# Kernel optimization log

Hardware: AMD Instinct MI355X
Metric: run time of the kernel (lower is better)

The kernel has to match this reference:

```python
import jax, jax.numpy as jnp
import numpy as np

B, T, C, H = 4, 2048, 1024, 16


def setup_inputs() -> dict:
    key = jax.random.key(0)
    k0, k1, k2 = jax.random.split(key, 3)
    s = C ** -0.5
    return {
        "x": jax.random.normal(k0, (B, T, C), jnp.float32),
        "Wqkv": jax.random.normal(k1, (C, 3 * C), jnp.float32) * s,
        "bqkv": jnp.zeros((3 * C,), jnp.float32),
        "Wo": jax.random.normal(k2, (C, C), jnp.float32) * s,
        "bo": jnp.zeros((C,), jnp.float32),
        "decoder": 1,
    }


def reference(x, Wqkv, bqkv, Wo, bo, decoder):
    Bx, Tx, Cx = x.shape
    d = Cx // H  # head dim
    qkv = x @ Wqkv + bqkv  # [B,T,3C]
    q, k, v = jnp.split(qkv, 3, axis=-1)
    q = q.reshape(Bx, Tx, H, d).transpose(0, 2, 1, 3)  # [B,H,T,d]
    k = k.reshape(Bx, Tx, H, d).transpose(0, 2, 1, 3)
    v = v.reshape(Bx, Tx, H, d).transpose(0, 2, 1, 3)
    # Source: qk / embd_dim**(-0.5)  ==  qk * sqrt(embd_dim)  (faithful quirk)
    scale = jnp.asarray(Cx ** 0.5, x.dtype)
    qk = jnp.einsum("bhqd,bhkd->bhqk", q, k) * scale  # [B,H,T,T]
    if decoder:  # decoder is a Python int constant
        tril = jnp.tril(jnp.ones((Tx, Tx), bool))
        qk = jnp.where(tril, qk, -jnp.inf)
    attn = jax.nn.softmax(qk, axis=-1)
    out = jnp.einsum("bhqk,bhkd->bhqd", attn, v)  # [B,H,T,d]
    out = out.transpose(0, 2, 1, 3).reshape(Bx, Tx, Cx)
    return out @ Wo + bo
```

## Files before the change

kernel.cpp:

```cpp
#include <hip/hip_runtime.h>
#include <cstdint>
#include <cstddef>

#define T_SEQ 2048
#define CEMB  1024
#define NHEAD 16
#define DHEAD 64

#define QSCALE 46.1662413084468f

typedef __attribute__((ext_vector_type(8))) short bf16x8;
typedef __attribute__((ext_vector_type(4))) float f32x4;

static __device__ __forceinline__ unsigned short f2bf(float x) {
    unsigned u = __builtin_bit_cast(unsigned, x);
    unsigned r = (u + 0x7FFFu + ((u >> 16) & 1u)) >> 16;
    return (unsigned short)r;
}
static __device__ __forceinline__ float bf2f(unsigned short b) {
    unsigned u = ((unsigned)b) << 16;
    return __builtin_bit_cast(float, u);
}

static __device__ __forceinline__ void gload16(const short* gsrc, short* ldsbase) {
    __builtin_amdgcn_global_load_lds(
        (const __attribute__((address_space(1))) void*)gsrc,
        (__attribute__((address_space(3))) void*)ldsbase, 16, 0, 0);
}

__global__ __launch_bounds__(256) void split_x_kernel(
    const float* __restrict__ x, short* __restrict__ hi, short* __restrict__ lo)
{
    size_t base = ((size_t)blockIdx.x * 256 + threadIdx.x) * 8;
    float4 f0 = *(const float4*)(x + base);
    float4 f1 = *(const float4*)(x + base + 4);
    float xs[8] = {f0.x, f0.y, f0.z, f0.w, f1.x, f1.y, f1.z, f1.w};
    bf16x8 h8, l8;
    #pragma unroll
    for (int e = 0; e < 8; ++e) {
        unsigned u = __builtin_bit_cast(unsigned, xs[e]);
        h8[e] = (short)(unsigned short)(u >> 16);
        float hf = __builtin_bit_cast(float, u & 0xFFFF0000u);
        l8[e] = (short)f2bf(xs[e] - hf);
    }
    *(bf16x8*)(hi + base) = h8;
    *(bf16x8*)(lo + base) = l8;
}

template<int SPLIT, int OUT_MODE>
__global__ __launch_bounds__(256) void gemm_mfma_kernel(
    const short* __restrict__ Ah, const short* __restrict__ Al,
    const short* __restrict__ Bh, const short* __restrict__ Bl,
    const float* __restrict__ bias,
    void* __restrict__ Cout, void* __restrict__ Cout2, int K, int ldc)
{
    __shared__ __align__(16) short smem[(SPLIT == 3) ? 16384 : 8192];

    const int tid = threadIdx.x;
    const int w = tid >> 6, l = tid & 63;
    const int lr = l & 15, lg = l >> 4;
    const int wr = w >> 1, wc = w & 1;
    const int row0 = blockIdx.y * 128;
    const int col0 = blockIdx.x * 128;

    f32x4 acc[4][4];
    #pragma unroll
    for (int mt = 0; mt < 4; ++mt)
        #pragma unroll
        for (int nt = 0; nt < 4; ++nt)
            acc[mt][nt] = (f32x4){0.f, 0.f, 0.f, 0.f};

    const int s0 = w * 128 + l, s1 = s0 + 64;
    const size_t aoff0 = (size_t)(row0 + (s0 & 127)) * K + (s0 >> 7) * 8;
    const size_t aoff1 = (size_t)(row0 + (s1 & 127)) * K + (s1 >> 7) * 8;
    const size_t boff0 = (size_t)(col0 + (s0 & 127)) * K + (s0 >> 7) * 8;
    const size_t boff1 = (size_t)(col0 + (s1 & 127)) * K + (s1 >> 7) * 8;
    const short* gA0 = Ah + aoff0;  const short* gA1 = Ah + aoff1;
    const short* gB0 = Bh + boff0;  const short* gB1 = Bh + boff1;
    const short* gAl0 = nullptr; const short* gAl1 = nullptr;
    const short* gBl0 = nullptr; const short* gBl1 = nullptr;
    if constexpr (SPLIT == 3) {
        gAl0 = Al + aoff0;  gAl1 = Al + aoff1;
        gBl0 = Bl + boff0;  gBl1 = Bl + boff1;
    }
    short* const dA0 = &smem[(w * 128) * 8];
    short* const dA1 = &smem[(w * 128 + 64) * 8];
    short* const dB0 = &smem[4096 + (w * 128) * 8];
    short* const dB1 = &smem[4096 + (w * 128 + 64) * 8];

    for (int kt = 0; kt < K; kt += 32) {
        __syncthreads();
        gload16(gA0 + kt, dA0);
        gload16(gA1 + kt, dA1);
        gload16(gB0 + kt, dB0);
        gload16(gB1 + kt, dB1);
        if constexpr (SPLIT == 3) {
            gload16(gAl0 + kt, dA0 + 8192);
            gload16(gAl1 + kt, dA1 + 8192);
            gload16(gBl0 + kt, dB0 + 8192);
            gload16(gBl1 + kt, dB1 + 8192);
        }
        __syncthreads();

        const int ao = (lg * 128 + wr * 64 + lr) * 8;
        const int bo = 4096 + (lg * 128 + wc * 64 + lr) * 8;
        bf16x8 ahf[4], alf[4];
        #pragma unroll
        for (int mt = 0; mt < 4; ++mt) {
            ahf[mt] = *(const bf16x8*)&smem[ao + mt * 128];
            if constexpr (SPLIT == 3)
                alf[mt] = *(const bf16x8*)&smem[8192 + ao + mt * 128];
        }
        #pragma unroll
        for (int nt = 0; nt < 4; ++nt) {
            bf16x8 bhf = *(const bf16x8*)&smem[bo + nt * 128];
            if constexpr (SPLIT == 3) {
                bf16x8 blf = *(const bf16x8*)&smem[8192 + bo + nt * 128];
                #pragma unroll
                for (int mt = 0; mt < 4; ++mt) {
                    acc[mt][nt] = __builtin_amdgcn_mfma_f32_16x16x32_bf16(ahf[mt], bhf, acc[mt][nt], 0, 0, 0);
                    acc[mt][nt] = __builtin_amdgcn_mfma_f32_16x16x32_bf16(alf[mt], bhf, acc[mt][nt], 0, 0, 0);
                    acc[mt][nt] = __builtin_amdgcn_mfma_f32_16x16x32_bf16(ahf[mt], blf, acc[mt][nt], 0, 0, 0);
                }
            } else {
                #pragma unroll
                for (int mt = 0; mt < 4; ++mt)
                    acc[mt][nt] = __builtin_amdgcn_mfma_f32_16x16x32_bf16(ahf[mt], bhf, acc[mt][nt], 0, 0, 0);
            }
        }
    }

    #pragma unroll
    for (int mt = 0; mt < 4; ++mt) {
        #pragma unroll
        for (int r = 0; r < 4; ++r) {
            int m = row0 + wr * 64 + mt * 16 + lg * 4 + r;
            #pragma unroll
            for (int nt = 0; nt < 4; ++nt) {
                int n = col0 + wc * 64 + nt * 16 + lr;
                float v = acc[mt][nt][r] + bias[n];
                if constexpr (OUT_MODE == 0) {
                    ((float*)Cout)[(size_t)m * ldc + n] = v;
                } else if constexpr (OUT_MODE == 1) {
                    ((short*)Cout)[(size_t)m * ldc + n] = (short)f2bf(v);
                } else {
                    if (n < 1024) v *= QSCALE;
                    unsigned u = __builtin_bit_cast(unsigned, v);
                    ((short*)Cout)[(size_t)m * ldc + n] = (short)(unsigned short)(u >> 16);
                    float hf = __builtin_bit_cast(float, u & 0xFFFF0000u);
                    ((short*)Cout2)[(size_t)m * ldc + n] = (short)f2bf(v - hf);
                }
            }
        }
    }
}

__global__ __launch_bounds__(256) void transpose_split_kernel(
    const float* __restrict__ src, int nsrc,
    short* __restrict__ hi, short* __restrict__ lo)
{
    __shared__ float tile[64][68];
    const int tid = threadIdx.x;
    const int n0 = blockIdx.x * 64, k0 = blockIdx.y * 64;
    {
        int kr = tid >> 2, cg = tid & 3;
        const float* s = src + (size_t)(k0 + kr) * nsrc + n0 + cg * 16;
        #pragma unroll
        for (int q = 0; q < 4; ++q) {
            float4 f = *(const float4*)(s + q * 4);
            tile[kr][cg * 16 + q * 4 + 0] = f.x;
            tile[kr][cg * 16 + q * 4 + 1] = f.y;
            tile[kr][cg * 16 + q * 4 + 2] = f.z;
            tile[kr][cg * 16 + q * 4 + 3] = f.w;
        }
    }
    __syncthreads();
    {
        int nr = tid >> 2, kg = tid & 3;
        int n = n0 + nr;
        bf16x8 h0, h1, lo0, lo1;
        #pragma unroll
        for (int e = 0; e < 8; ++e) {
            float a = tile[kg * 16 + e][nr];
            float b = tile[kg * 16 + 8 + e][nr];
            unsigned short ha = f2bf(a), hb = f2bf(b);
            h0[e] = (short)ha; h1[e] = (short)hb;
            lo0[e] = (short)f2bf(a - bf2f(ha));
            lo1[e] = (short)f2bf(b - bf2f(hb));
        }
        short* dh = hi + (size_t)n * 1024 + k0 + kg * 16;
        *(bf16x8*)dh = h0;
        *(bf16x8*)(dh + 8) = h1;
        if (lo) {
            short* dl = lo + (size_t)n * 1024 + k0 + kg * 16;
            *(bf16x8*)dl = lo0;
            *(bf16x8*)(dl + 8) = lo1;
        }
    }
}

__global__ __launch_bounds__(256) void repack_vt_kernel(
    const short* __restrict__ v, short* __restrict__ vt)
{
    __shared__ short tile[64][80];
    const int tid = threadIdx.x;
    const int tt = blockIdx.x, h = blockIdx.y, b = blockIdx.z;
    const int t0 = tt * 64;
    {
        int tr = tid >> 2, cgrp = tid & 3;
        const short* src = v + (size_t)(b * T_SEQ + t0 + tr) * CEMB + h * DHEAD + cgrp * 16;
        *(bf16x8*)&tile[tr][cgrp * 16]     = *(const bf16x8*)src;
        *(bf16x8*)&tile[tr][cgrp * 16 + 8] = *(const bf16x8*)(src + 8);
    }
    __syncthreads();
    {
        int d = tid >> 2, tc = tid & 3;
        short s[16];
        #pragma unroll
        for (int e = 0; e < 16; ++e) s[e] = tile[tc * 16 + e][d];
        short* dst = vt + ((size_t)((b * NHEAD + h) * DHEAD + d)) * T_SEQ + t0 + tc * 16;
        bf16x8 v0, v1;
        #pragma unroll
        for (int e = 0; e < 8; ++e) { v0[e] = s[e]; v1[e] = s[8 + e]; }
        *(bf16x8*)dst       = v0;
        *(bf16x8*)(dst + 8) = v1;
    }
}

__global__ __launch_bounds__(256) void attn_mfma_kernel(
    const short* __restrict__ qkhi, const short* __restrict__ qklo,
    const short* __restrict__ vt, short* __restrict__ ctxb)
{
    __shared__ __align__(16) short smem[20480];

    const int tid = threadIdx.x;
    const int w = tid >> 6, l = tid & 63;
    const int lr = l & 15, lg = l >> 4;

    const int bid = blockIdx.x;
    const int p  = bid >> 6;
    const int bh = bid & 63;
    const int h = bh & 15, b = bh >> 4;
    const size_t bT = (size_t)b * T_SEQ;

    const int g0 = w * 128 + l, g1 = g0 + 64;
    const int rg0 = g0 >> 3, rg1 = g1 >> 3;
    const int sc0 = (g0 & 7) ^ (rg0 & 7), sc1 = (g1 & 7) ^ (rg1 & 7);
    short* const dK0 = &smem[(w * 128) * 8];
    short* const dK1 = &smem[(w * 128 + 64) * 8];

    const size_t koff0 = (bT + rg0) * 2048 + 1024 + h * DHEAD + sc0 * 8;
    const size_t koff1 = (bT + rg1) * 2048 + 1024 + h * DHEAD + sc1 * 8;
    const short* const pKh0 = qkhi + koff0;
    const short* const pKh1 = qkhi + koff1;
    const short* const pKl0 = qklo + koff0;
    const short* const pKl1 = qklo + koff1;
    const short* const pV0 = vt + ((size_t)((b * NHEAD + h) * DHEAD) + rg0) * T_SEQ + sc0 * 8;
    const short* const pV1 = vt + ((size_t)((b * NHEAD + h) * DHEAD) + rg1) * T_SEQ + sc1 * 8;

    const int psBase = 16384 + w * 1024;
    const int pwChunk = (lg >> 1);
    const int pwIntra = (lg & 1) * 4;

    for (int half = 0; half < 2; ++half) {
        const int xi = half ? (31 - p) : p;
        const int qw = xi * 64 + w * 16;
        const int nsteps = xi + 1;

        __syncthreads();

        bf16x8 qhi[2], qlo[2];
        #pragma unroll
        for (int kk = 0; kk < 2; ++kk) {
            size_t off = (bT + qw + lr) * 2048 + h * DHEAD + kk * 32 + lg * 8;
            qhi[kk] = *(const bf16x8*)(qkhi + off);
            qlo[kk] = *(const bf16x8*)(qklo + off);
        }
        __builtin_amdgcn_sched_barrier(0);

        gload16(pKh0, dK0);
        gload16(pKh1, dK1);
        gload16(pKl0, dK0 + 4096);
        gload16(pKl1, dK1 + 4096);
        gload16(pV0, dK0 + 8192);
        gload16(pV1, dK1 + 8192);
        {
            int j1 = (nsteps > 1) ? 64 : 0;
            gload16(pV0 + j1, dK0 + 12288);
            gload16(pV1 + j1, dK1 + 12288);
        }

        f32x4 O[4];
        #pragma unroll
        for (int dt = 0; dt < 4; ++dt)
            O[dt] = (f32x4){0.f, 0.f, 0.f, 0.f};
        float mrow = -3.0e38f;
        float lrow = 0.f;

        for (int t = 0; t < nsteps; ++t) {
            const int j0 = t * 64;
            asm volatile("s_waitcnt vmcnt(2)" ::: "memory");
            __builtin_amdgcn_s_barrier();
            __builtin_amdgcn_sched_barrier(0);
            const int vbase = 8192 + (t & 1) * 4096;

            f32x4 St[4];
            __builtin_amdgcn_s_setprio(1);
            #pragma unroll
            for (int ct = 0; ct < 4; ++ct) {
                f32x4 s = (f32x4){0.f, 0.f, 0.f, 0.f};
                #pragma unroll
                for (int kk = 0; kk < 2; ++kk) {
                    int j  = ct * 16 + lr;
                    int ck = kk * 4 + lg;
                    int idx = j * 64 + ((ck ^ (j & 7)) << 3);
                    bf16x8 kh8 = *(bf16x8*)&smem[idx];
                    bf16x8 kl8 = *(bf16x8*)&smem[4096 + idx];
                    s = __builtin_amdgcn_mfma_f32_16x16x32_bf16(kh8, qhi[kk], s, 0, 0, 0);
                    s = __builtin_amdgcn_mfma_f32_16x16x32_bf16(kh8, qlo[kk], s, 0, 0, 0);
                    s = __builtin_amdgcn_mfma_f32_16x16x32_bf16(kl8, qhi[kk], s, 0, 0, 0);
                }
                St[ct] = s;
            }
            __builtin_amdgcn_s_setprio(0);
            #pragma unroll
            for (int ct = 0; ct < 4; ++ct) {
                if (j0 + ct * 16 + 15 > qw) {
                    #pragma unroll
                    for (int r = 0; r < 4; ++r) {
                        int jabs = j0 + ct * 16 + lg * 4 + r;
                        St[ct][r] = (jabs <= qw + lr) ? St[ct][r] : -3.0e38f;
                    }
                }
            }

            float tm = fmaxf(fmaxf(fmaxf(St[0][0], St[0][1]), fmaxf(St[0][2], St[0][3])),
                             fmaxf(fmaxf(St[1][0], St[1][1]), fmaxf(St[1][2], St[1][3])));
            tm = fmaxf(tm, fmaxf(fmaxf(fmaxf(St[2][0], St[2][1]), fmaxf(St[2][2], St[2][3])),
                                 fmaxf(fmaxf(St[3][0], St[3][1]), fmaxf(St[3][2], St[3][3]))));
            tm = fmaxf(tm, __shfl_xor(tm, 16));
            tm = fmaxf(tm, __shfl_xor(tm, 32));

            if (__any(tm > mrow)) {
                float mnew  = fmaxf(mrow, tm);
                float alpha = __builtin_amdgcn_exp2f(mrow - mnew);
                mrow = mnew;
                lrow *= alpha;
                #pragma unroll
                for (int r = 0; r < 4; ++r) {
                    float aO = __shfl(alpha, lg * 4 + r);
                    #pragma unroll
                    for (int dt = 0; dt < 4; ++dt)
                        O[dt][r] *= aO;
                }
            }

            #pragma unroll
            for (int ct = 0; ct < 4; ++ct) {
                float p0 = __builtin_amdgcn_exp2f(St[ct][0] - mrow);
                float p1 = __builtin_amdgcn_exp2f(St[ct][1] - mrow);
                float p2 = __builtin_amdgcn_exp2f(St[ct][2] - mrow);
                float p3 = __builtin_amdgcn_exp2f(St[ct][3] - mrow);
                lrow += (p0 + p1) + (p2 + p3);
                unsigned u0 = (__builtin_bit_cast(unsigned, p0) >> 16) |
                              (__builtin_bit_cast(unsigned, p1) & 0xFFFF0000u);
                unsigned u1 = (__builtin_bit_cast(unsigned, p2) >> 16) |
                              (__builtin_bit_cast(unsigned, p3) & 0xFFFF0000u);
                int chunk = ct * 2 + pwChunk;
                int sidx = psBase + lr * 64 + ((chunk ^ (lr & 7)) << 3) + pwIntra;
                uint2 uu; uu.x = u0; uu.y = u1;
                *(uint2*)&smem[sidx] = uu;
            }

            __builtin_amdgcn_wave_barrier();

            bf16x8 pa[2];
            #pragma unroll
            for (int jk = 0; jk < 2; ++jk) {
                int ck = jk * 4 + lg;
                pa[jk] = *(bf16x8*)&smem[psBase + lr * 64 + ((ck ^ (lr & 7)) << 3)];
            }
            __builtin_amdgcn_s_setprio(1);
            #pragma unroll
            for (int dt = 0; dt < 4; ++dt) {
                #pragma unroll
                for (int jk = 0; jk < 2; ++jk) {
                    int d  = dt * 16 + lr;
                    int ck = jk * 4 + lg;
                    bf16x8 vb = *(bf16x8*)&smem[vbase + d * 64 + ((ck ^ (d & 7)) << 3)];
                    O[dt] = __builtin_amdgcn_mfma_f32_16x16x32_bf16(pa[jk], vb, O[dt], 0, 0, 0);
                }
            }
            __builtin_amdgcn_s_setprio(0);

            __builtin_amdgcn_sched_barrier(0);
            __builtin_amdgcn_s_barrier();
            __builtin_amdgcn_sched_barrier(0);

            if (t + 1 < nsteps) {
                size_t ko = (size_t)(t + 1) * 131072;
                gload16(pKh0 + ko, dK0);
                gload16(pKh1 + ko, dK1);
                gload16(pKl0 + ko, dK0 + 4096);
                gload16(pKl1 + ko, dK1 + 4096);
                int jv = (t + 2 < nsteps) ? (t + 2) : (nsteps - 1);
                short* const dV = &smem[8192 + (t & 1) * 4096];
                gload16(pV0 + jv * 64, dV + (w * 128) * 8);
                gload16(pV1 + jv * 64, dV + (w * 128 + 64) * 8);
            }
        }

        float lsum = lrow + __shfl_xor(lrow, 16);
        lsum += __shfl_xor(lsum, 32);
        #pragma unroll
        for (int r = 0; r < 4; ++r) {
            float lO = __shfl(lsum, lg * 4 + r);
            float inv = 1.0f / lO;
            int row = qw + lg * 4 + r;
            #pragma unroll
            for (int dt = 0; dt < 4; ++dt) {
                int col = h * DHEAD + dt * 16 + lr;
                ctxb[(size_t)(b * T_SEQ + row) * CEMB + col] = (short)f2bf(O[dt][r] * inv);
            }
        }
    }
}

extern "C" void kernel_launch(void* const* d_in, const int* in_sizes, int n_in,
                              void* d_out, int out_size, void* d_ws, size_t ws_size,
                              hipStream_t stream)
{
    const float* x    = (const float*)d_in[0];
    const float* Wqkv = (const float*)d_in[1];
    const float* bqkv = (const float*)d_in[2];
    const float* Wo   = (const float*)d_in[3];
    const float* bo   = (const float*)d_in[4];
    float* out = (float*)d_out;

    char* ws = (char*)d_ws;
    short* qkhi = (short*)ws;
    short* qklo = (short*)(ws + (size_t)(32u << 20));
    short* xlo  = (short*)(ws + (size_t)(64u << 20));
    short* vbuf = xlo;
    short* ctxb = xlo;
    short* xhi  = (short*)(ws + (size_t)(80u << 20));
    short* Vt   = xhi;
    short* WhiT = (short*)(ws + (size_t)(96u << 20));
    short* WloT = (short*)(ws + (size_t)(102u << 20));
    short* WoT  = (short*)(ws + (size_t)(108u << 20));

    transpose_split_kernel<<<dim3(48, 16), 256, 0, stream>>>(Wqkv, 3 * CEMB, WhiT, WloT);
    transpose_split_kernel<<<dim3(16, 16), 256, 0, stream>>>(Wo, CEMB, WoT, nullptr);

    split_x_kernel<<<dim3(4096), 256, 0, stream>>>(x, xhi, xlo);

    gemm_mfma_kernel<3, 2><<<dim3(16, 64), 256, 0, stream>>>(
        xhi, xlo, WhiT, WloT, bqkv, qkhi, qklo, CEMB, 2048);

    gemm_mfma_kernel<1, 1><<<dim3(8, 64), 256, 0, stream>>>(
        xhi, nullptr, WhiT + (size_t)2048 * 1024, nullptr, bqkv + 2048,
        vbuf, nullptr, CEMB, CEMB);

    repack_vt_kernel<<<dim3(32, 16, 4), 256, 0, stream>>>(vbuf, Vt);

    attn_mfma_kernel<<<dim3(1024), 256, 0, stream>>>(qkhi, qklo, Vt, ctxb);

    gemm_mfma_kernel<1, 0><<<dim3(8, 64), 256, 0, stream>>>(
        ctxb, nullptr, WoT, nullptr, bo, out, nullptr, CEMB, CEMB);
}
```

Baseline: 359.4 us.

## Fuse V transpose into V GEMM epilogue and enlarge QK GEMM tiles

Splits the templated GEMM into three specialized kernels. The V projection now writes its result transposed straight into the per-head Vt layout by staging it through shared memory, so the separate repack kernel and its extra round trip through global memory are gone. The split-precision QK GEMM moves to 512-thread blocks with 256-row tiles, so each B tile is reused across twice as many rows. The cost is more shared memory and registers per block, which may lower occupancy, and the workspace buffers are reassigned.

```diff
diff --git a/kernel.cpp b/kernel.cpp
--- a/kernel.cpp
+++ b/kernel.cpp
@@ -47,14 +47,97 @@
     *(bf16x8*)(lo + base) = l8;
 }
 
-template<int SPLIT, int OUT_MODE>
-__global__ __launch_bounds__(256) void gemm_mfma_kernel(
+__global__ __launch_bounds__(512) void gemm_qk_kernel(
     const short* __restrict__ Ah, const short* __restrict__ Al,
     const short* __restrict__ Bh, const short* __restrict__ Bl,
     const float* __restrict__ bias,
-    void* __restrict__ Cout, void* __restrict__ Cout2, int K, int ldc)
-{
-    __shared__ __align__(16) short smem[(SPLIT == 3) ? 16384 : 8192];
+    short* __restrict__ Chi, short* __restrict__ Clo, int K)
+{
+    __shared__ __align__(16) short smem[24576];
+
+    const int tid = threadIdx.x;
+    const int wv = tid >> 6, l = tid & 63;
+    const int lr = l & 15, lg = l >> 4;
+    const int wr = wv >> 1, wc = wv & 1;
+    const int row0 = blockIdx.y * 256;
+    const int col0 = blockIdx.x * 128;
+
+    f32x4 acc[4][4];
+    #pragma unroll
+    for (int mt = 0; mt < 4; ++mt)
+        #pragma unroll
+        for (int nt = 0; nt < 4; ++nt)
+            acc[mt][nt] = (f32x4){0.f, 0.f, 0.f, 0.f};
+
+    const int sA0 = wv * 128 + l, sA1 = sA0 + 64;
+    const size_t aO0 = (size_t)(row0 + (sA0 & 255)) * K + (sA0 >> 8) * 8;
+    const size_t aO1 = (size_t)(row0 + (sA1 & 255)) * K + (sA1 >> 8) * 8;
+    const int sB = wv * 64 + l;
+    const size_t bO = (size_t)(col0 + (sB & 127)) * K + (sB >> 7) * 8;
+
+    const short* gAh0 = Ah + aO0;  const short* gAh1 = Ah + aO1;
+    const short* gAl0 = Al + aO0;  const short* gAl1 = Al + aO1;
+    const short* gBh  = Bh + bO;   const short* gBl  = Bl + bO;
+
+    short* const dA0 = &smem[(wv * 128) * 8];
+    short* const dA1 = &smem[(wv * 128 + 64) * 8];
+    short* const dB  = &smem[16384 + (wv * 64) * 8];
+
+    for (int kt = 0; kt < K; kt += 32) {
+        __syncthreads();
+        gload16(gAh0 + kt, dA0);
+        gload16(gAh1 + kt, dA1);
+        gload16(gAl0 + kt, dA0 + 8192);
+        gload16(gAl1 + kt, dA1 + 8192);
+        gload16(gBh + kt, dB);
+        gload16(gBl + kt, dB + 4096);
+        __syncthreads();
+
+        const int ao = (lg * 256 + wr * 64 + lr) * 8;
+        const int bo = 16384 + (lg * 128 + wc * 64 + lr) * 8;
+        bf16x8 ahf[4], alf[4];
+        #pragma unroll
+        for (int mt = 0; mt < 4; ++mt) {
+            ahf[mt] = *(const bf16x8*)&smem[ao + mt * 128];
+            alf[mt] = *(const bf16x8*)&smem[8192 + ao + mt * 128];
+        }
+        #pragma unroll
+        for (int nt = 0; nt < 4; ++nt) {
+            bf16x8 bhf = *(const bf16x8*)&smem[bo + nt * 128];
+            bf16x8 blf = *(const bf16x8*)&smem[4096 + bo + nt * 128];
+            #pragma unroll
+            for (int mt = 0; mt < 4; ++mt) {
+                acc[mt][nt] = __builtin_amdgcn_mfma_f32_16x16x32_bf16(ahf[mt], bhf, acc[mt][nt], 0, 0, 0);
+                acc[mt][nt] = __builtin_amdgcn_mfma_f32_16x16x32_bf16(alf[mt], bhf, acc[mt][nt], 0, 0, 0);
+                acc[mt][nt] = __builtin_amdgcn_mfma_f32_16x16x32_bf16(ahf[mt], blf, acc[mt][nt], 0, 0, 0);
+            }
+        }
+    }
+
+    #pragma unroll
+    for (int mt = 0; mt < 4; ++mt) {
+        #pragma unroll
+        for (int r = 0; r < 4; ++r) {
+            int m = row0 + wr * 64 + mt * 16 + lg * 4 + r;
+            #pragma unroll
+            for (int nt = 0; nt < 4; ++nt) {
+                int n = col0 + wc * 64 + nt * 16 + lr;
+                float v = acc[mt][nt][r] + bias[n];
+                if (n < 1024) v *= QSCALE;
+                unsigned u = __builtin_bit_cast(unsigned, v);
+                Chi[(size_t)m * 2048 + n] = (short)(unsigned short)(u >> 16);
+                float hf = __builtin_bit_cast(float, u & 0xFFFF0000u);
+                Clo[(size_t)m * 2048 + n] = (short)f2bf(v - hf);
+            }
+        }
+    }
+}
+
+__global__ __launch_bounds__(256) void gemm_v_kernel(
+    const short* __restrict__ Ah, const short* __restrict__ Bh,
+    const float* __restrict__ bias, short* __restrict__ vt, int K)
+{
+    __shared__ __align__(16) short smem[17408];
 
     const int tid = threadIdx.x;
     const int w = tid >> 6, l = tid & 63;
@@ -77,12 +160,6 @@
     const size_t boff1 = (size_t)(col0 + (s1 & 127)) * K + (s1 >> 7) * 8;
     const short* gA0 = Ah + aoff0;  const short* gA1 = Ah + aoff1;
     const short* gB0 = Bh + boff0;  const short* gB1 = Bh + boff1;
-    const short* gAl0 = nullptr; const short* gAl1 = nullptr;
-    const short* gBl0 = nullptr; const short* gBl1 = nullptr;
-    if constexpr (SPLIT == 3) {
-        gAl0 = Al + aoff0;  gAl1 = Al + aoff1;
-        gBl0 = Bl + boff0;  gBl1 = Bl + boff1;
-    }
     short* const dA0 = &smem[(w * 128) * 8];
     short* const dA1 = &smem[(w * 128 + 64) * 8];
     short* const dB0 = &smem[4096 + (w * 128) * 8];
@@ -94,39 +171,108 @@
         gload16(gA1 + kt, dA1);
         gload16(gB0 + kt, dB0);
         gload16(gB1 + kt, dB1);
-        if constexpr (SPLIT == 3) {
-            gload16(gAl0 + kt, dA0 + 8192);
-            gload16(gAl1 + kt, dA1 + 8192);
-            gload16(gBl0 + kt, dB0 + 8192);
-            gload16(gBl1 + kt, dB1 + 8192);
-        }
         __syncthreads();
 
         const int ao = (lg * 128 + wr * 64 + lr) * 8;
         const int bo = 4096 + (lg * 128 + wc * 64 + lr) * 8;
-        bf16x8 ahf[4], alf[4];
-        #pragma unroll
-        for (int mt = 0; mt < 4; ++mt) {
+        bf16x8 ahf[4];
+        #pragma unroll
+        for (int mt = 0; mt < 4; ++mt)
             ahf[mt] = *(const bf16x8*)&smem[ao + mt * 128];
-            if constexpr (SPLIT == 3)
-                alf[mt] = *(const bf16x8*)&smem[8192 + ao + mt * 128];
-        }
         #pragma unroll
         for (int nt = 0; nt < 4; ++nt) {
             bf16x8 bhf = *(const bf16x8*)&smem[bo + nt * 128];
-            if constexpr (SPLIT == 3) {
-                bf16x8 blf = *(const bf16x8*)&smem[8192 + bo + nt * 128];
-                #pragma unroll
-                for (int mt = 0; mt < 4; ++mt) {
-                    acc[mt][nt] = __builtin_amdgcn_mfma_f32_16x16x32_bf16(ahf[mt], bhf, acc[mt][nt], 0, 0, 0);
-                    acc[mt][nt] = __builtin_amdgcn_mfma_f32_16x16x32_bf16(alf[mt], bhf, acc[mt][nt], 0, 0, 0);
-                    acc[mt][nt] = __builtin_amdgcn_mfma_f32_16x16x32_bf16(ahf[mt], blf, acc[mt][nt], 0, 0, 0);
-                }
-            } else {
-                #pragma unroll
-                for (int mt = 0; mt < 4; ++mt)
-                    acc[mt][nt] = __builtin_amdgcn_mfma_f32_16x16x32_bf16(ahf[mt], bhf, acc[mt][nt], 0, 0, 0);
-            }
+            #pragma unroll
+            for (int mt = 0; mt < 4; ++mt)
+                acc[mt][nt] = __builtin_amdgcn_mfma_f32_16x16x32_bf16(ahf[mt], bhf, acc[mt][nt], 0, 0, 0);
+        }
+    }
+
+    __syncthreads();
+    #pragma unroll
+    for (int mt = 0; mt < 4; ++mt) {
+        const int tb = wr * 64 + mt * 16 + lg * 4;
+        #pragma unroll
+        for (int nt = 0; nt < 4; ++nt) {
+            const int nl = wc * 64 + nt * 16 + lr;
+            float v0 = acc[mt][nt][0] + bias[col0 + nl];
+            float v1 = acc[mt][nt][1] + bias[col0 + nl];
+            float v2 = acc[mt][nt][2] + bias[col0 + nl];
+            float v3 = acc[mt][nt][3] + bias[col0 + nl];
+            unsigned u0 = (unsigned)f2bf(v0) | ((unsigned)f2bf(v1) << 16);
+            unsigned u1 = (unsigned)f2bf(v2) | ((unsigned)f2bf(v3) << 16);
+            uint2 uu; uu.x = u0; uu.y = u1;
+            *(uint2*)&smem[nl * 136 + tb] = uu;
+        }
+    }
+    __syncthreads();
+
+    const int b  = row0 >> 11;
+    const int t0 = row0 & 2047;
+    #pragma unroll
+    for (int i = 0; i < 8; ++i) {
+        int nl = (tid >> 4) + i * 16;
+        int t8 = (tid & 15) * 8;
+        bf16x8 vv = *(const bf16x8*)&smem[nl * 136 + t8];
+        int n = col0 + nl;
+        int hh = n >> 6, d = n & 63;
+        short* dst = vt + ((size_t)((b * NHEAD + hh) * DHEAD + d)) * T_SEQ + t0 + t8;
+        *(bf16x8*)dst = vv;
+    }
+}
+
+__global__ __launch_bounds__(256) void gemm_proj_kernel(
+    const short* __restrict__ Ah, const short* __restrict__ Bh,
+    const float* __restrict__ bias, float* __restrict__ Cout, int K, int ldc)
+{
+    __shared__ __align__(16) short smem[8192];
+
+    const int tid = threadIdx.x;
+    const int w = tid >> 6, l = tid & 63;
+    const int lr = l & 15, lg = l >> 4;
+    const int wr = w >> 1, wc = w & 1;
+    const int row0 = blockIdx.y * 128;
+    const int col0 = blockIdx.x * 128;
+
+    f32x4 acc[4][4];
+    #pragma unroll
+    for (int mt = 0; mt < 4; ++mt)
+        #pragma unroll
+        for (int nt = 0; nt < 4; ++nt)
+            acc[mt][nt] = (f32x4){0.f, 0.f, 0.f, 0.f};
+
+    const int s0 = w * 128 + l, s1 = s0 + 64;
+    const size_t aoff0 = (size_t)(row0 + (s0 & 127)) * K + (s0 >> 7) * 8;
+    const size_t aoff1 = (size_t)(row0 + (s1 & 127)) * K + (s1 >> 7) * 8;
+    const size_t boff0 = (size_t)(col0 + (s0 & 127)) * K + (s0 >> 7) * 8;
+    const size_t boff1 = (size_t)(col0 + (s1 & 127)) * K + (s1 >> 7) * 8;
+    const short* gA0 = Ah + aoff0;  const short* gA1 = Ah + aoff1;
+    const short* gB0 = Bh + boff0;  const short* gB1 = Bh + boff1;
+    short* const dA0 = &smem[(w * 128) * 8];
+    short* const dA1 = &smem[(w * 128 + 64) * 8];
+    short* const dB0 = &smem[4096 + (w * 128) * 8];
+    short* const dB1 = &smem[4096 + (w * 128 + 64) * 8];
+
+    for (int kt = 0; kt < K; kt += 32) {
+        __syncthreads();
+        gload16(gA0 + kt, dA0);
+        gload16(gA1 + kt, dA1);
+        gload16(gB0 + kt, dB0);
+        gload16(gB1 + kt, dB1);
+        __syncthreads();
+
+        const int ao = (lg * 128 + wr * 64 + lr) * 8;
+        const int bo = 4096 + (lg * 128 + wc * 64 + lr) * 8;
+        bf16x8 ahf[4];
+        #pragma unroll
+        for (int mt = 0; mt < 4; ++mt)
+            ahf[mt] = *(const bf16x8*)&smem[ao + mt * 128];
+        #pragma unroll
+        for (int nt = 0; nt < 4; ++nt) {
+            bf16x8 bhf = *(const bf16x8*)&smem[bo + nt * 128];
+            #pragma unroll
+            for (int mt = 0; mt < 4; ++mt)
+                acc[mt][nt] = __builtin_amdgcn_mfma_f32_16x16x32_bf16(ahf[mt], bhf, acc[mt][nt], 0, 0, 0);
         }
     }
 
@@ -138,18 +284,7 @@
             #pragma unroll
             for (int nt = 0; nt < 4; ++nt) {
                 int n = col0 + wc * 64 + nt * 16 + lr;
-                float v = acc[mt][nt][r] + bias[n];
-                if constexpr (OUT_MODE == 0) {
-                    ((float*)Cout)[(size_t)m * ldc + n] = v;
-                } else if constexpr (OUT_MODE == 1) {
-                    ((short*)Cout)[(size_t)m * ldc + n] = (short)f2bf(v);
-                } else {
-                    if (n < 1024) v *= QSCALE;
-                    unsigned u = __builtin_bit_cast(unsigned, v);
-                    ((short*)Cout)[(size_t)m * ldc + n] = (short)(unsigned short)(u >> 16);
-                    float hf = __builtin_bit_cast(float, u & 0xFFFF0000u);
-                    ((short*)Cout2)[(size_t)m * ldc + n] = (short)f2bf(v - hf);
-                }
+                Cout[(size_t)m * ldc + n] = acc[mt][nt][r] + bias[n];
             }
         }
     }
@@ -196,34 +331,6 @@
             *(bf16x8*)dl = lo0;
             *(bf16x8*)(dl + 8) = lo1;
         }
-    }
-}
-
-__global__ __launch_bounds__(256) void repack_vt_kernel(
-    const short* __restrict__ v, short* __restrict__ vt)
-{
-    __shared__ short tile[64][80];
-    const int tid = threadIdx.x;
-    const int tt = blockIdx.x, h = blockIdx.y, b = blockIdx.z;
-    const int t0 = tt * 64;
-    {
-        int tr = tid >> 2, cgrp = tid & 3;
-        const short* src = v + (size_t)(b * T_SEQ + t0 + tr) * CEMB + h * DHEAD + cgrp * 16;
-        *(bf16x8*)&tile[tr][cgrp * 16]     = *(const bf16x8*)src;
-        *(bf16x8*)&tile[tr][cgrp * 16 + 8] = *(const bf16x8*)(src + 8);
-    }
-    __syncthreads();
-    {
-        int d = tid >> 2, tc = tid & 3;
-        short s[16];
-        #pragma unroll
-        for (int e = 0; e < 16; ++e) s[e] = tile[tc * 16 + e][d];
-        short* dst = vt + ((size_t)((b * NHEAD + h) * DHEAD + d)) * T_SEQ + t0 + tc * 16;
-        bf16x8 v0, v1;
-        #pragma unroll
-        for (int e = 0; e < 8; ++e) { v0[e] = s[e]; v1[e] = s[8 + e]; }
-        *(bf16x8*)dst       = v0;
-        *(bf16x8*)(dst + 8) = v1;
     }
 }
 
@@ -441,10 +548,9 @@
     short* qkhi = (short*)ws;
     short* qklo = (short*)(ws + (size_t)(32u << 20));
     short* xlo  = (short*)(ws + (size_t)(64u << 20));
-    short* vbuf = xlo;
-    short* ctxb = xlo;
+    short* Vt   = xlo;
     short* xhi  = (short*)(ws + (size_t)(80u << 20));
-    short* Vt   = xhi;
+    short* ctxb = xhi;
     short* WhiT = (short*)(ws + (size_t)(96u << 20));
     short* WloT = (short*)(ws + (size_t)(102u << 20));
     short* WoT  = (short*)(ws + (size_t)(108u << 20));
@@ -454,17 +560,14 @@
 
     split_x_kernel<<<dim3(4096), 256, 0, stream>>>(x, xhi, xlo);
 
-    gemm_mfma_kernel<3, 2><<<dim3(16, 64), 256, 0, stream>>>(
-        xhi, xlo, WhiT, WloT, bqkv, qkhi, qklo, CEMB, 2048);
-
-    gemm_mfma_kernel<1, 1><<<dim3(8, 64), 256, 0, stream>>>(
-        xhi, nullptr, WhiT + (size_t)2048 * 1024, nullptr, bqkv + 2048,
-        vbuf, nullptr, CEMB, CEMB);
-
-    repack_vt_kernel<<<dim3(32, 16, 4), 256, 0, stream>>>(vbuf, Vt);
+    gemm_qk_kernel<<<dim3(16, 32), 512, 0, stream>>>(
+        xhi, xlo, WhiT, WloT, bqkv, qkhi, qklo, CEMB);
+
+    gemm_v_kernel<<<dim3(8, 64), 256, 0, stream>>>(
+        xhi, WhiT + (size_t)2048 * 1024, bqkv + 2048, Vt, CEMB);
 
     attn_mfma_kernel<<<dim3(1024), 256, 0, stream>>>(qkhi, qklo, Vt, ctxb);
 
-    gemm_mfma_kernel<1, 0><<<dim3(8, 64), 256, 0, stream>>>(
-        ctxb, nullptr, WoT, nullptr, bo, out, nullptr, CEMB, CEMB);
-}
+    gemm_proj_kernel<<<dim3(8, 64), 256, 0, stream>>>(
+        ctxb, WoT, bo, out, CEMB, CEMB);
+}
```

After: 395.3 us. +10.0%, slower.
